# Kernel tuning notes

Hardware: AMD Instinct MI355X
Metric: run time of the kernel (lower is better)

## Reference

```python
import jax, jax.numpy as jnp
import numpy as np

B, N, E, H, X, K = 8, 1024, 1024, 1536, 8, 2  # batch, seq, emb, hidden, experts, top-k


def setup_inputs() -> dict:
    key = jax.random.key(0)
    ks = jax.random.split(key, 4)
    s = 0.02
    return {
        "x": jax.random.normal(ks[0], (B, N, E), dtype=jnp.float32),
        "W_router": (jax.random.normal(ks[1], (E, X), dtype=jnp.float32) * s),
        "b_router": jnp.zeros((X,), dtype=jnp.float32),
        "W1": (jax.random.normal(ks[2], (X, E, H), dtype=jnp.float32) * s),
        "b1": jnp.zeros((X, H), dtype=jnp.float32),
        "W2": (jax.random.normal(ks[3], (X, H, E), dtype=jnp.float32) * s),
        "b2": jnp.zeros((X, E), dtype=jnp.float32),
    }


def reference(x, W_router, b_router, W1, b1, W2, b2):
    # x: [B, N, E]. Dropout is identity at inference (p irrelevant).
    Bb, Nn, Ee = x.shape
    scores = jax.nn.softmax(x @ W_router + b_router, axis=-1)      # [B, N, X]
    topk_vals, topk_idx = jax.lax.top_k(scores, K)                 # [B, N, K]
    flat_x = x.reshape(Bb * Nn, Ee)                                # [T, E]
    # Dense all-expert compute, matching torch.stack over experts.
    h = jnp.einsum('te,xeh->txh', flat_x, W1) + b1                 # [T, X, H]
    h = jax.nn.gelu(h, approximate=False)                          # torch GELU default = erf
    expert_out = jnp.einsum('txh,xhe->txe', h, W2) + b2            # [T, X, E]
    flat_idx = topk_idx.reshape(Bb * Nn, K)                        # [T, K]
    topk_outs = jnp.take_along_axis(expert_out, flat_idx[:, :, None], axis=1)  # [T, K, E]
    out = topk_outs.reshape(Bb, Nn, K, Ee).mean(axis=2)            # [B, N, E]
    return out, topk_idx
```

## Files before the change

### kernel.cpp

```cpp
#include <hip/hip_runtime.h>
#include <hip/hip_bf16.h>
#include <math.h>

#define T_TOK 8192
#define E_DIM 1024
#define H_DIM 1536
#define X_EXP 8

typedef unsigned short u16;
typedef unsigned int u32;

typedef __attribute__((ext_vector_type(8))) short frag_ab;
typedef __attribute__((ext_vector_type(4))) float frag_cd;

__device__ __forceinline__ u16 f2bf(float f) {
  u32 u = __float_as_uint(f);
  u32 r = u + 0x7fffu + ((u >> 16) & 1u);
  return (u16)(r >> 16);
}
__device__ __forceinline__ float bf2f(u16 h) {
  return __uint_as_float(((u32)h) << 16);
}

__device__ __forceinline__ void gl2lds16(const u16* g, u16* l) {
  __builtin_amdgcn_global_load_lds((const __attribute__((address_space(1))) void*)g,
                                   (__attribute__((address_space(3))) void*)l,
                                   16, 0, 0);
}

static const size_t O_T2    = 4096;
static const size_t O_CLIST = O_T2 + (size_t)T_TOK * 2 * 4;
static const size_t O_XB    = O_CLIST + (size_t)T_TOK * 2 * 4;
static const size_t O_W1T   = O_XB + (size_t)T_TOK * E_DIM * 2;
static const size_t O_W2T   = O_W1T + (size_t)X_EXP * E_DIM * H_DIM * 2;
static const size_t O_HB    = O_W2T + (size_t)X_EXP * E_DIM * H_DIM * 2;
static const size_t O_Y     = O_XB;

__global__ __launch_bounds__(256) void k_prep(const float* __restrict__ x,
                                              const float* __restrict__ Wr,
                                              const float* __restrict__ br,
                                              const float* __restrict__ W1,
                                              const float* __restrict__ W2,
                                              float* __restrict__ out,
                                              u16* __restrict__ xb,
                                              u16* __restrict__ w1t,
                                              u16* __restrict__ w2t,
                                              int* __restrict__ t2,
                                              int* __restrict__ counts) {
  __shared__ union {
    float tile[64][65];
    struct { float red[4][4][8]; int cnt[8]; } r;
  } sm;
  int blk = blockIdx.x;
  int tid = threadIdx.x;

  if (blk < 256) {
    float4 wq[8];
    {
      const float4* wr4 = (const float4*)Wr + (size_t)tid * 8;
#pragma unroll
      for (int j = 0; j < 8; j++) wq[j] = wr4[j];
    }
    if (tid < 8) sm.r.cnt[tid] = 0;
    __syncthreads();

    int lane = tid & 63, wave = tid >> 6;
    for (int chunk = 0; chunk < 8; chunk++) {
      int tbase = blk * 32 + chunk * 4;
      float acc[4][8];
#pragma unroll
      for (int it = 0; it < 4; it++)
#pragma unroll
        for (int e = 0; e < 8; e++) acc[it][e] = 0.f;

#pragma unroll
      for (int it = 0; it < 4; it++) {
        size_t base = (size_t)(tbase + it) * 1024 + tid * 4;
        float4 v = *(const float4*)(x + base);
        ushort4 o;
        o.x = f2bf(v.x); o.y = f2bf(v.y); o.z = f2bf(v.z); o.w = f2bf(v.w);
        *(ushort4*)(xb + base) = o;
        float xv[4] = {v.x, v.y, v.z, v.w};
#pragma unroll
        for (int j = 0; j < 4; j++) {
#pragma unroll
          for (int e = 0; e < 8; e++) {
            float4 q = wq[j * 2 + (e >> 2)];
            float wv = (e & 3) == 0 ? q.x : (e & 3) == 1 ? q.y : (e & 3) == 2 ? q.z : q.w;
            acc[it][e] += xv[j] * wv;
          }
        }
      }
#pragma unroll
      for (int off = 32; off; off >>= 1)
#pragma unroll
        for (int it = 0; it < 4; it++)
#pragma unroll
          for (int e = 0; e < 8; e++)
            acc[it][e] += __shfl_down(acc[it][e], off);
      if (lane == 0) {
#pragma unroll
        for (int it = 0; it < 4; it++)
#pragma unroll
          for (int e = 0; e < 8; e++) sm.r.red[wave][it][e] = acc[it][e];
      }
      __syncthreads();
      if (tid < 4) {
        int t = tbase + tid;
        float lg[8];
#pragma unroll
        for (int e = 0; e < 8; e++)
          lg[e] = sm.r.red[0][tid][e] + sm.r.red[1][tid][e] + sm.r.red[2][tid][e] + sm.r.red[3][tid][e] + br[e];
        int i0 = 0; float v0 = lg[0];
#pragma unroll
        for (int e = 1; e < 8; e++) if (lg[e] > v0) { v0 = lg[e]; i0 = e; }
        int i1 = -1; float v1 = -3.4e38f;
#pragma unroll
        for (int e = 0; e < 8; e++) if (e != i0 && lg[e] > v1) { v1 = lg[e]; i1 = e; }
        out[(size_t)T_TOK * E_DIM + (size_t)t * 2 + 0] = (float)i0;
        out[(size_t)T_TOK * E_DIM + (size_t)t * 2 + 1] = (float)i1;
        t2[t * 2 + 0] = i0;
        t2[t * 2 + 1] = i1;
        atomicAdd(&sm.r.cnt[i0], 1);
        atomicAdd(&sm.r.cnt[i1], 1);
      }
      __syncthreads();
    }
    if (tid < 8) atomicAdd(&counts[tid], sm.r.cnt[tid]);
  } else {
    const float* src; u16* dst; int R, C, bx, by, e;
    if (blk < 256 + 3072) {
      int l = blk - 256;
      bx = l % 24; by = (l / 24) % 16; e = l / 384;
      R = E_DIM; C = H_DIM;
      src = W1 + (size_t)e * R * C; dst = w1t + (size_t)e * R * C;
    } else {
      int l = blk - (256 + 3072);
      bx = l % 16; by = (l / 16) % 24; e = l / 384;
      R = H_DIM; C = E_DIM;
      src = W2 + (size_t)e * R * C; dst = w2t + (size_t)e * R * C;
    }
    int c0 = bx * 64, r0 = by * 64;
    int tc = tid & 15, tr = tid >> 4;
#pragma unroll
    for (int i = 0; i < 4; i++) {
      int rr = tr + i * 16;
      float4 v = *(const float4*)(src + (size_t)(r0 + rr) * C + c0 + tc * 4);
      sm.tile[rr][tc * 4 + 0] = v.x;
      sm.tile[rr][tc * 4 + 1] = v.y;
      sm.tile[rr][tc * 4 + 2] = v.z;
      sm.tile[rr][tc * 4 + 3] = v.w;
    }
    __syncthreads();
#pragma unroll
    for (int i = 0; i < 4; i++) {
      int hh = tr + i * 16;
      ushort4 o;
      o.x = f2bf(sm.tile[tc * 4 + 0][hh]);
      o.y = f2bf(sm.tile[tc * 4 + 1][hh]);
      o.z = f2bf(sm.tile[tc * 4 + 2][hh]);
      o.w = f2bf(sm.tile[tc * 4 + 3][hh]);
      *(ushort4*)(dst + (size_t)(c0 + hh) * R + r0 + tc * 4) = o;
    }
  }
}

__global__ __launch_bounds__(256) void k_fill(int* __restrict__ t2,
                                              const int* __restrict__ counts,
                                              int* __restrict__ curs,
                                              int* __restrict__ clist) {
  __shared__ int c8[8], base8[8];
  int tid = threadIdx.x;
  if (tid < 8) c8[tid] = 0;
  __syncthreads();

  int t = blockIdx.x * 256 + tid;
  int e0 = t2[t * 2 + 0] & 7;
  int e1 = t2[t * 2 + 1] & 7;
  int r0 = atomicAdd(&c8[e0], 1);
  int r1 = atomicAdd(&c8[e1], 1);
  __syncthreads();
  if (tid < 8) base8[tid] = atomicAdd(&curs[tid], c8[tid]);
  __syncthreads();

  int offs[8];
  {
    int run = 0;
#pragma unroll
    for (int e = 0; e < 8; e++) { offs[e] = run; run += counts[e]; }
  }
  int s0 = offs[e0] + base8[e0] + r0;
  int s1 = offs[e1] + base8[e1] + r1;
  clist[s0] = t;
  clist[s1] = t;
  t2[t * 2 + 0] = e0 | (s0 << 3);
  t2[t * 2 + 1] = e1 | (s1 << 3);
}


#define STG_A(cc, kk, ss) gl2lds16(gA[ss] + (kk), lA + (cc) * LDSTILE + ((ss) * 512 + tid) * 8)
#define STG_B(cc, kk, ss) gl2lds16(gB[ss] + (kk), lB + (cc) * LDSTILE + ((ss) * 512 + tid) * 8)
#define LDA8(qm) { const u16* cA_ = lA + c * LDSTILE; \
  _Pragma("unroll") for (int i_ = 0; i_ < 4; i_++) { \
    const u16* p_ = cA_ + (wm * 128 + ((qm) * 4 + i_) * 16 + mr) * 64; \
    Af[i_ * 2 + 0] = *(const frag_ab*)(p_ + g0); \
    Af[i_ * 2 + 1] = *(const frag_ab*)(p_ + g1); } }
#define LDB4(qn) { const u16* cB_ = lB + c * LDSTILE; \
  _Pragma("unroll") for (int j_ = 0; j_ < 2; j_++) { \
    const u16* p_ = cB_ + (wn * 64 + ((qn) * 2 + j_) * 16 + mr) * 64; \
    Bf[j_ * 2 + 0] = *(const frag_ab*)(p_ + g0); \
    Bf[j_ * 2 + 1] = *(const frag_ab*)(p_ + g1); } }
#define MMA16(qm, qn) { \
  _Pragma("unroll") for (int i_ = 0; i_ < 4; i_++) \
  _Pragma("unroll") for (int j_ = 0; j_ < 2; j_++) { \
    acc[(qm) * 4 + i_][(qn) * 2 + j_] = __builtin_amdgcn_mfma_f32_16x16x32_bf16(Af[i_ * 2 + 0], Bf[j_ * 2 + 0], acc[(qm) * 4 + i_][(qn) * 2 + j_], 0, 0, 0); \
    acc[(qm) * 4 + i_][(qn) * 2 + j_] = __builtin_amdgcn_mfma_f32_16x16x32_bf16(Af[i_ * 2 + 1], Bf[j_ * 2 + 1], acc[(qm) * 4 + i_][(qn) * 2 + j_], 0, 0, 0); } }
#define WAITLGKM do { asm volatile("s_waitcnt lgkmcnt(0)" ::: "memory"); \
  __builtin_amdgcn_sched_barrier(0); } while (0)

template<int KD, int CN, bool GELU, bool GATHER>
__global__ __launch_bounds__(512, 2) void k_gemm8(const u16* __restrict__ Ag,
                                                  const u16* __restrict__ Bw,
                                                  const float* __restrict__ bias,
                                                  u16* __restrict__ Cg,
                                                  const int* __restrict__ counts,
                                                  const int* __restrict__ clist) {
  constexpr int NTI = CN / 256;
  constexpr int NKT = KD / 64;
  constexpr int MT  = 12;
  constexpr int LDSTILE = 256 * 64;
  int bid = blockIdx.x;
  int e = bid & 7;
  int slot = bid >> 3;
  int cnt = counts[e];
  int mt = slot / NTI;
  int n0 = (slot % NTI) * 256;
  int off = 0;
#pragma unroll
  for (int j = 0; j < 8; j++) off += (j < e) ? counts[j] : 0;

  int tid = threadIdx.x;
  int lane = tid & 63, wave = tid >> 6;
  int wm = wave >> 2, wn = wave & 3;

  extern __shared__ __align__(16) u16 sm8[];
  u16* lA = sm8;
  u16* lB = sm8 + 2 * LDSTILE;

  int q = lane >> 4, mr = lane & 15;
  int g0 = (q ^ (mr & 7)) * 8;
  int g1 = g0 ^ (4 * 8);

  for (int m0 = mt * 256; m0 < cnt; m0 += MT * 256) {
    const u16* gA[4];
    const u16* gB[4];
#pragma unroll
    for (int s = 0; s < 4; s++) {
      int idx = s * 512 + tid;
      int r = idx >> 3;
      int cg = (idx & 7) ^ (r & 7);
      int mrow = m0 + r; if (mrow >= cnt) mrow = cnt - 1;
      size_t arow;
      if constexpr (GATHER) arow = (size_t)clist[off + mrow] * KD;
      else                  arow = (size_t)(off + mrow) * KD;
      gA[s] = Ag + arow + cg * 8;
      gB[s] = Bw + (size_t)e * CN * KD + (size_t)(n0 + r) * KD + cg * 8;
    }

    frag_cd acc[8][4] = {};
    frag_ab Af[8], Bf[4];

#pragma unroll
    for (int s = 0; s < 4; s++) STG_A(0, 0, s);
#pragma unroll
    for (int s = 0; s < 4; s++) STG_B(0, 0, s);

#pragma unroll 2
    for (int t = 0; t < NKT; t++) {
      int c = t & 1;
      int kn = (t + 1) * 64;
      bool pf = (t + 1) < NKT;
      if (pf) {
        STG_A(c ^ 1, kn, 0); STG_A(c ^ 1, kn, 1);
        asm volatile("s_waitcnt vmcnt(2)" ::: "memory");
      } else {
        asm volatile("s_waitcnt vmcnt(0)" ::: "memory");
      }
      __builtin_amdgcn_s_barrier();
      LDA8(0); LDB4(0);
      if (pf) { STG_A(c ^ 1, kn, 2); STG_A(c ^ 1, kn, 3); }
      WAITLGKM;
      __builtin_amdgcn_s_setprio(1);
      MMA16(0, 0);
      __builtin_amdgcn_s_setprio(0);
      __builtin_amdgcn_s_barrier();
      LDB4(1);
      if (pf) { STG_B(c ^ 1, kn, 0); STG_B(c ^ 1, kn, 1); }
      WAITLGKM;
      __builtin_amdgcn_s_setprio(1);
      MMA16(0, 1);
      __builtin_amdgcn_s_setprio(0);
      __builtin_amdgcn_s_barrier();
      LDA8(1);
      if (pf) { STG_B(c ^ 1, kn, 2); STG_B(c ^ 1, kn, 3); }
      WAITLGKM;
      __builtin_amdgcn_s_setprio(1);
      MMA16(1, 1);
      __builtin_amdgcn_s_setprio(0);
      __builtin_amdgcn_s_barrier();
      LDB4(0);
      WAITLGKM;
      __builtin_amdgcn_s_setprio(1);
      MMA16(1, 0);
      __builtin_amdgcn_s_setprio(0);
      __builtin_amdgcn_s_barrier();
    }

#pragma unroll
    for (int fi = 0; fi < 8; fi++) {
#pragma unroll
      for (int fj = 0; fj < 4; fj++) {
        int ng = n0 + wn * 64 + fj * 16 + mr;
        float bv = 0.f;
        if constexpr (GELU) bv = bias[e * CN + ng];
#pragma unroll
        for (int r = 0; r < 4; r++) {
          int mg = m0 + wm * 128 + fi * 16 + q * 4 + r;
          if (mg < cnt) {
            float v = acc[fi][fj][r];
            if constexpr (GELU) {
              v += bv;
              float z = v * (1.5957691216f + 0.0713548162f * v * v);
              v = v / (1.0f + __expf(-z));
            }
            Cg[(size_t)(off + mg) * CN + ng] = f2bf(v);
          }
        }
      }
    }
  }
}

__global__ __launch_bounds__(256) void k_combine(const u16* __restrict__ y,
                                                 const float* __restrict__ b2,
                                                 const int* __restrict__ t2,
                                                 float* __restrict__ out) {
  int t = blockIdx.x;
  int c = threadIdx.x * 4;
  int v0 = t2[t * 2 + 0], v1 = t2[t * 2 + 1];
  int e0 = v0 & 7, s0 = v0 >> 3;
  int e1 = v1 & 7, s1 = v1 >> 3;
  ushort4 a = *(const ushort4*)(y + (size_t)s0 * E_DIM + c);
  ushort4 b = *(const ushort4*)(y + (size_t)s1 * E_DIM + c);
  float4 p0 = *(const float4*)(b2 + (size_t)e0 * E_DIM + c);
  float4 p1 = *(const float4*)(b2 + (size_t)e1 * E_DIM + c);
  float4 o;
  o.x = 0.5f * (bf2f(a.x) + bf2f(b.x) + p0.x + p1.x);
  o.y = 0.5f * (bf2f(a.y) + bf2f(b.y) + p0.y + p1.y);
  o.z = 0.5f * (bf2f(a.z) + bf2f(b.z) + p0.z + p1.z);
  o.w = 0.5f * (bf2f(a.w) + bf2f(b.w) + p0.w + p1.w);
  *(float4*)(out + (size_t)t * E_DIM + c) = o;
}

extern "C" void kernel_launch(void* const* d_in, const int* in_sizes, int n_in,
                              void* d_out, int out_size, void* d_ws, size_t ws_size,
                              hipStream_t stream) {
  (void)in_sizes; (void)n_in; (void)out_size; (void)ws_size;
  const float* x  = (const float*)d_in[0];
  const float* Wr = (const float*)d_in[1];
  const float* br = (const float*)d_in[2];
  const float* W1 = (const float*)d_in[3];
  const float* b1 = (const float*)d_in[4];
  const float* W2 = (const float*)d_in[5];
  const float* b2 = (const float*)d_in[6];
  float* out = (float*)d_out;
  char* ws = (char*)d_ws;

  int* meta  = (int*)ws;
  int* t2    = (int*)(ws + O_T2);
  int* clist = (int*)(ws + O_CLIST);
  u16* xb    = (u16*)(ws + O_XB);
  u16* w1t   = (u16*)(ws + O_W1T);
  u16* w2t   = (u16*)(ws + O_W2T);
  u16* hb    = (u16*)(ws + O_HB);
  u16* y     = (u16*)(ws + O_Y);

  static int attr_once = [] {
    (void)hipFuncSetAttribute(reinterpret_cast<const void*>(&k_gemm8<E_DIM, H_DIM, true, true>),
                              hipFuncAttributeMaxDynamicSharedMemorySize, 131072);
    (void)hipFuncSetAttribute(reinterpret_cast<const void*>(&k_gemm8<H_DIM, E_DIM, false, false>),
                              hipFuncAttributeMaxDynamicSharedMemorySize, 131072);
    return 0;
  }();
  (void)attr_once;

  hipMemsetAsync(ws, 0, 128, stream);

  k_prep<<<dim3(256 + 3072 + 3072), 256, 0, stream>>>(x, Wr, br, W1, W2, out, xb, w1t, w2t, t2, meta);
  k_fill<<<dim3(T_TOK / 256), 256, 0, stream>>>(t2, meta, meta + 16, clist);
  k_gemm8<E_DIM, H_DIM, true, true><<<dim3(8 * 12 * 6), 512, 131072, stream>>>(
      xb, w1t, b1, hb, meta, clist);
  k_gemm8<H_DIM, E_DIM, false, false><<<dim3(8 * 12 * 4), 512, 131072, stream>>>(
      hb, w2t, nullptr, y, meta, nullptr);
  k_combine<<<dim3(T_TOK), 256, 0, stream>>>(y, b2, t2, out);
}
```

Before: 369.2 us.

## Convert weights to bf16 before LDS transpose, move GEMM barriers, cut tile grid

The weight-transpose prep now converts to bf16 as values are loaded and stores a bf16 tile in LDS. Each thread then writes 16 contiguous bf16 per row with wide stores, which shrinks LDS traffic and widens the global writes. In the grouped GEMM the barriers move to sit just before each LDS-wait and MMA group rather than after it. The per-expert M-tile count drops from 12 to 8, giving smaller grids. If MT bounds the per-expert row tiles, experts holding more than 2048 routed tokens could be left uncovered, so correctness depends on how MT is used.

```diff
diff --git a/kernel.cpp b/kernel.cpp
--- a/kernel.cpp
+++ b/kernel.cpp
@@ -48,7 +48,7 @@
                                               int* __restrict__ t2,
                                               int* __restrict__ counts) {
   __shared__ union {
-    float tile[64][65];
+    u16 lt[64][76];
     struct { float red[4][4][8]; int cnt[8]; } r;
   } sm;
   int blk = blockIdx.x;
@@ -142,25 +142,29 @@
     }
     int c0 = bx * 64, r0 = by * 64;
     int tc = tid & 15, tr = tid >> 4;
-#pragma unroll
-    for (int i = 0; i < 4; i++) {
-      int rr = tr + i * 16;
-      float4 v = *(const float4*)(src + (size_t)(r0 + rr) * C + c0 + tc * 4);
-      sm.tile[rr][tc * 4 + 0] = v.x;
-      sm.tile[rr][tc * 4 + 1] = v.y;
-      sm.tile[rr][tc * 4 + 2] = v.z;
-      sm.tile[rr][tc * 4 + 3] = v.w;
+    {
+      float4 v0 = *(const float4*)(src + (size_t)(r0 + tr * 4 + 0) * C + c0 + tc * 4);
+      float4 v1 = *(const float4*)(src + (size_t)(r0 + tr * 4 + 1) * C + c0 + tc * 4);
+      float4 v2 = *(const float4*)(src + (size_t)(r0 + tr * 4 + 2) * C + c0 + tc * 4);
+      float4 v3 = *(const float4*)(src + (size_t)(r0 + tr * 4 + 3) * C + c0 + tc * 4);
+      ushort4 w;
+      w.x = f2bf(v0.x); w.y = f2bf(v1.x); w.z = f2bf(v2.x); w.w = f2bf(v3.x);
+      *(ushort4*)(&sm.lt[tc * 4 + 0][tr * 4]) = w;
+      w.x = f2bf(v0.y); w.y = f2bf(v1.y); w.z = f2bf(v2.y); w.w = f2bf(v3.y);
+      *(ushort4*)(&sm.lt[tc * 4 + 1][tr * 4]) = w;
+      w.x = f2bf(v0.z); w.y = f2bf(v1.z); w.z = f2bf(v2.z); w.w = f2bf(v3.z);
+      *(ushort4*)(&sm.lt[tc * 4 + 2][tr * 4]) = w;
+      w.x = f2bf(v0.w); w.y = f2bf(v1.w); w.z = f2bf(v2.w); w.w = f2bf(v3.w);
+      *(ushort4*)(&sm.lt[tc * 4 + 3][tr * 4]) = w;
     }
     __syncthreads();
-#pragma unroll
-    for (int i = 0; i < 4; i++) {
-      int hh = tr + i * 16;
-      ushort4 o;
-      o.x = f2bf(sm.tile[tc * 4 + 0][hh]);
-      o.y = f2bf(sm.tile[tc * 4 + 1][hh]);
-      o.z = f2bf(sm.tile[tc * 4 + 2][hh]);
-      o.w = f2bf(sm.tile[tc * 4 + 3][hh]);
-      *(ushort4*)(dst + (size_t)(c0 + hh) * R + r0 + tc * 4) = o;
+    {
+      int cc = tid >> 2, rs = (tid & 3) * 16;
+      frag_ab a = *(const frag_ab*)(&sm.lt[cc][rs]);
+      frag_ab b = *(const frag_ab*)(&sm.lt[cc][rs + 8]);
+      u16* drow = dst + (size_t)(c0 + cc) * R + r0 + rs;
+      *(frag_ab*)(drow) = a;
+      *(frag_ab*)(drow + 8) = b;
     }
   }
 }
@@ -227,7 +231,7 @@
                                                   const int* __restrict__ clist) {
   constexpr int NTI = CN / 256;
   constexpr int NKT = KD / 64;
-  constexpr int MT  = 12;
+  constexpr int MT  = 8;
   constexpr int LDSTILE = 256 * 64;
   int bid = blockIdx.x;
   int e = bid & 7;
@@ -289,26 +293,27 @@
       __builtin_amdgcn_s_barrier();
       LDA8(0); LDB4(0);
       if (pf) { STG_A(c ^ 1, kn, 2); STG_A(c ^ 1, kn, 3); }
+      __builtin_amdgcn_s_barrier();
       WAITLGKM;
       __builtin_amdgcn_s_setprio(1);
       MMA16(0, 0);
       __builtin_amdgcn_s_setprio(0);
-      __builtin_amdgcn_s_barrier();
       LDB4(1);
       if (pf) { STG_B(c ^ 1, kn, 0); STG_B(c ^ 1, kn, 1); }
+      __builtin_amdgcn_s_barrier();
       WAITLGKM;
       __builtin_amdgcn_s_setprio(1);
       MMA16(0, 1);
       __builtin_amdgcn_s_setprio(0);
-      __builtin_amdgcn_s_barrier();
       LDA8(1);
       if (pf) { STG_B(c ^ 1, kn, 2); STG_B(c ^ 1, kn, 3); }
+      __builtin_amdgcn_s_barrier();
       WAITLGKM;
       __builtin_amdgcn_s_setprio(1);
       MMA16(1, 1);
       __builtin_amdgcn_s_setprio(0);
-      __builtin_amdgcn_s_barrier();
       LDB4(0);
+      __builtin_amdgcn_s_barrier();
       WAITLGKM;
       __builtin_amdgcn_s_setprio(1);
       MMA16(1, 0);
@@ -398,9 +403,9 @@
 
   k_prep<<<dim3(256 + 3072 + 3072), 256, 0, stream>>>(x, Wr, br, W1, W2, out, xb, w1t, w2t, t2, meta);
   k_fill<<<dim3(T_TOK / 256), 256, 0, stream>>>(t2, meta, meta + 16, clist);
-  k_gemm8<E_DIM, H_DIM, true, true><<<dim3(8 * 12 * 6), 512, 131072, stream>>>(
+  k_gemm8<E_DIM, H_DIM, true, true><<<dim3(8 * 8 * 6), 512, 131072, stream>>>(
       xb, w1t, b1, hb, meta, clist);
-  k_gemm8<H_DIM, E_DIM, false, false><<<dim3(8 * 12 * 4), 512, 131072, stream>>>(
+  k_gemm8<H_DIM, E_DIM, false, false><<<dim3(8 * 8 * 4), 512, 131072, stream>>>(
       hb, w2t, nullptr, y, meta, nullptr);
   k_combine<<<dim3(T_TOK), 256, 0, stream>>>(y, b2, t2, out);
 }
```

Measured after the change: 369.1 us. Within noise of the previous version (-0.0%).
